# Kernel tuning notes

Measured on AMD Instinct MI355X. Metric: run time of the kernel, lower is better.

The kernel has to match this reference:

```python
import jax, jax.numpy as jnp
import numpy as np

B, F, T = 2, 512, 512
D, N, H = 1024, 16, 64   # hidden, heads, head_dim
K = 32                   # time-bias MLP kernal_size
FILT = 4096              # FFN filter size
L = 4                    # num_decoder_blocks
EPS = 1e-6


def _glorot(key, shape, fan_in, fan_out):
    lim = np.sqrt(6.0 / (fan_in + fan_out)).astype(np.float32)
    return jax.random.uniform(key, shape, jnp.float32, -lim, lim)


def setup_inputs() -> dict:
    key = jax.random.key(0)
    ks = jax.random.split(key, 18)
    inp = {
        'decoder_inputs': jax.random.normal(ks[0], (B, F, D), jnp.float32),
        'encoder_outputs': jax.random.normal(ks[1], (B, T, D), jnp.float32),
        'decoder_times_dist': jax.random.uniform(ks[2], (B, F, F), jnp.float32),
        'decoder_encoder_times_dist': jax.random.uniform(ks[3], (B, F, T), jnp.float32),
        'dec_self_attn_bias': jnp.zeros((B, 1, 1, F), jnp.float32),
        'enc_dec_attn_bias': jnp.zeros((B, 1, 1, T), jnp.float32),
        # per-block stacked parameters (leading dim L)
        'Wq': _glorot(ks[4], (L, D, N, H), D, D),
        'Wk': _glorot(ks[5], (L, D, N, H), D, D),
        'Wv': _glorot(ks[6], (L, D, N, H), D, D),
        'Wo': _glorot(ks[7], (L, N, H, D), D, D),
        'Wth': _glorot(ks[8], (L, 1, K), 1, K),
        'bth': jnp.zeros((L, K), jnp.float32),
        'Wto': _glorot(ks[9], (L, K, 1), K, 1),
        'bto': jnp.zeros((L, 1), jnp.float32),
        'Wf1': _glorot(ks[10], (L, D, FILT), D, FILT),
        'bf1': jnp.zeros((L, FILT), jnp.float32),
        'Wf2': _glorot(ks[11], (L, FILT, D), FILT, D),
        'bf2': jnp.zeros((L, D), jnp.float32),
    }
    return inp


def _norm(x):
    # non-trainable LayerNormalization: (x - mean) / (std + eps)
    m = jnp.mean(x, axis=-1, keepdims=True)
    s = jnp.sqrt(jnp.mean((x - m) ** 2, axis=-1, keepdims=True))
    return (x - m) / (s + EPS)


def _attention(x, src, dist, bias, Wq, Wk, Wv, Wo, Wth, bth, Wto, bto):
    q = jnp.einsum('bfd,dnh->bfnh', x, Wq) * (H ** -0.5)
    k = jnp.einsum('btd,dnh->btnh', src, Wk)
    v = jnp.einsum('btd,dnh->btnh', src, Wv)
    # learned time bias: [B,F,T,1] -> relu MLP(K) -> 1 -> [B,F,T]
    hbias = jax.nn.relu(dist[..., None] @ Wth + bth)        # [B,F,T,K]
    qs_bias = (hbias @ Wto + bto)[..., 0]                   # [B,F,T]
    logits = jnp.einsum('btnh,bfnh->bnft', k, q)            # [B,N,F,T]
    logits = logits + bias + qs_bias[:, None]
    w = jax.nn.softmax(logits, axis=-1)
    out = jnp.einsum('bnft,btnh->bfnh', w, v)
    return jnp.einsum('bfnh,nhd->bfd', out, Wo)


def reference(decoder_inputs, encoder_outputs, decoder_times_dist,
              decoder_encoder_times_dist, dec_self_attn_bias, enc_dec_attn_bias,
              Wq, Wk, Wv, Wo, Wth, bth, Wto, bto, Wf1, bf1, Wf2, bf2):
    # decoder_times_dist / dec_self_attn_bias are accepted but unused (as in source call)
    x = decoder_inputs
    for i in range(L):
        # enc-dec attention with pre-norm + residual
        y = _attention(_norm(x), encoder_outputs, decoder_encoder_times_dist,
                       enc_dec_attn_bias, Wq[i], Wk[i], Wv[i], Wo[i],
                       Wth[i], bth[i], Wto[i], bto[i])
        x = x + y
        # FFN with pre-norm + residual
        y = jax.nn.relu(_norm(x) @ Wf1[i] + bf1[i]) @ Wf2[i] + bf2[i]
        x = x + y
    return _norm(x)
```

## Files before the change

kernel.cpp:

```cpp
#include <hip/hip_runtime.h>

typedef unsigned short u16;
typedef __attribute__((ext_vector_type(8))) unsigned short u16x8;
typedef __attribute__((ext_vector_type(4))) unsigned short u16x4;
typedef __attribute__((ext_vector_type(4))) float f32x4;

#define DEVI __device__ __forceinline__

DEVI u16 f2bf(float f){
  unsigned u = __float_as_uint(f);
  u += 0x7FFFu + ((u >> 16) & 1u);
  return (u16)(u >> 16);
}

DEVI float bf2f(u16 b){
  return __uint_as_float((unsigned)b << 16);
}

DEVI void gload16(const void* g, void* l){
  __builtin_amdgcn_global_load_lds((const __attribute__((address_space(1))) void*)g,
                                   (__attribute__((address_space(3))) void*)l, 16, 0, 0);
}

DEVI float wave_sum(float v){
#pragma unroll
  for (int o = 32; o; o >>= 1) v += __shfl_xor(v, o, 64);
  return v;
}

#define MFMA16(a,b,c) __builtin_amdgcn_mfma_f32_16x16x32_bf16((a),(b),(c),0,0,0)

__global__ __launch_bounds__(256) void prep_k(
    const float* __restrict__ Wq, const float* __restrict__ Wk,
    const float* __restrict__ Wv, const float* __restrict__ Wo,
    const float* __restrict__ Wf1, const float* __restrict__ Wf2,
    const float* __restrict__ enc, const float* __restrict__ dist,
    const float* __restrict__ Wth0, const float* __restrict__ bth0,
    const float* __restrict__ Wto0, const float* __restrict__ bto0,
    u16* __restrict__ Wqt, u16* __restrict__ Wkt,
    u16* __restrict__ Wvt, u16* __restrict__ Wot,
    u16* __restrict__ Wf1t, u16* __restrict__ Wf2t,
    u16* __restrict__ encb, u16* __restrict__ qs0){
  __shared__ float tile[64][65];
  const int t = blockIdx.x;
  if (t < 12288){
    const float* in; u16* out; int R, C, r0, c0;
    if (t < 4096){
      const int mat = t >> 8, ti = t & 255, sel = mat >> 2, l = mat & 3;
      in  = (sel == 0 ? Wq : sel == 1 ? Wk : sel == 2 ? Wv : Wo) + (size_t)l * 1048576;
      out = (sel == 0 ? Wqt : sel == 1 ? Wkt : sel == 2 ? Wvt : Wot) + (size_t)l * 1048576;
      R = 1024; C = 1024; r0 = (ti & 15) << 6; c0 = (ti >> 4) << 6;
    } else if (t < 8192){
      const int t2 = t - 4096, mat = t2 >> 10, ti = t2 & 1023;
      in = Wf1 + (size_t)mat * 4194304; out = Wf1t + (size_t)mat * 4194304;
      R = 1024; C = 4096; r0 = (ti & 15) << 6; c0 = (ti >> 4) << 6;
    } else {
      const int t2 = t - 8192, mat = t2 >> 10, ti = t2 & 1023;
      in = Wf2 + (size_t)mat * 4194304; out = Wf2t + (size_t)mat * 4194304;
      R = 4096; C = 1024; r0 = (ti & 63) << 6; c0 = (ti >> 6) << 6;
    }
    const int rr0 = threadIdx.x >> 4, cc = (threadIdx.x & 15) * 4;
#pragma unroll
    for (int it = 0; it < 4; it++){
      const int rr = rr0 + it * 16;
      const float4 v = *(const float4*)(in + (size_t)(r0 + rr) * C + c0 + cc);
      tile[rr][cc] = v.x; tile[rr][cc+1] = v.y;
      tile[rr][cc+2] = v.z; tile[rr][cc+3] = v.w;
    }
    __syncthreads();
#pragma unroll
    for (int it = 0; it < 2; it++){
      const int chunk = threadIdx.x + it * 256;
      const int c = chunk >> 3, q = (chunk & 7) * 8;
      union { u16x8 v8; u16 e[8]; } ob;
#pragma unroll
      for (int i = 0; i < 8; i++) ob.e[i] = f2bf(tile[q + i][c]);
      *(u16x8*)(out + (size_t)(c0 + c) * R + r0 + q) = ob.v8;
    }
  } else if (t < 13312){
    const int i = (t - 12288) * 256 + threadIdx.x;
    float4 v = ((const float4*)enc)[i];
    u16x4 o = { f2bf(v.x), f2bf(v.y), f2bf(v.z), f2bf(v.w) };
    ((u16x4*)encb)[i] = o;
  } else {
    const int bi = t - 13312, ly = bi >> 9, xi = bi & 511;
    const float* Wth = Wth0 + ly*32;
    const float* bth = bth0 + ly*32;
    const float* Wto = Wto0 + ly*32;
    u16* qs = qs0 + (size_t)ly * 524288;
    const int idx = xi * 256 + threadIdx.x;
    float4 s4 = ((const float4*)dist)[idx];
    float sv[4] = { s4.x, s4.y, s4.z, s4.w };
    float r[4];
    const float b0 = bto0[ly];
#pragma unroll
    for (int c = 0; c < 4; c++) r[c] = b0;
#pragma unroll
    for (int k = 0; k < 32; k++){
      const float wk = Wth[k], bk = bth[k], ok = Wto[k];
#pragma unroll
      for (int c = 0; c < 4; c++){
        float h = fmaxf(sv[c] * wk + bk, 0.0f);
        r[c] += h * ok;
      }
    }
    u16x4 o = { f2bf(r[0]), f2bf(r[1]), f2bf(r[2]), f2bf(r[3]) };
    ((u16x4*)qs)[idx] = o;
  }
}

template<int COPY>
__global__ __launch_bounds__(256) void layernorm_k(const float* __restrict__ in,
                                                   float* __restrict__ x,
                                                   u16* __restrict__ outp){
  const int row = blockIdx.x;
  const int tid = threadIdx.x;
  const float4 v = ((const float4*)(in + (size_t)row * 1024))[tid];
  if (COPY) ((float4*)x)[(size_t)row * 256 + tid] = v;
  __shared__ float sb[8];
  const int wid = tid >> 6, lane = tid & 63;
  float s = wave_sum(v.x + v.y + v.z + v.w);
  if (lane == 0) sb[wid] = s;
  __syncthreads();
  const float mean = (sb[0] + sb[1] + sb[2] + sb[3]) * (1.0f / 1024.0f);
  const float dx = v.x - mean, dy = v.y - mean, dz = v.z - mean, dw = v.w - mean;
  float q = wave_sum(dx*dx + dy*dy + dz*dz + dw*dw);
  if (lane == 0) sb[4 + wid] = q;
  __syncthreads();
  const float sd = sqrtf((sb[4] + sb[5] + sb[6] + sb[7]) * (1.0f / 1024.0f));
  const float inv = 1.0f / (sd + 1e-6f);
  u16x4 o = { f2bf(dx*inv), f2bf(dy*inv), f2bf(dz*inv), f2bf(dw*inv) };
  ((u16x4*)outp)[(size_t)row * 256 + tid] = o;
}

template<int MODE, int BN>
DEVI void gemm128_core(const u16* A, int lda, const u16* Bt, int ldb,
                       int Klen, int Nd, void* Cout,
                       const float* bias, u16* Als, u16* Bls, int row0, int col0){
  constexpr int WN = BN / 2, FN = BN / 32;
  constexpr int BSZ = BN * 64;
  const int tid = threadIdx.x;
  const int wid = tid >> 6, lane = tid & 63;
  const int wm = wid >> 1, wn = wid & 1;
  const int lrow = lane & 15, g = lane >> 4, e7 = lane & 7;
  f32x4 acc[4][FN] = {};

  const int scol = ((lane & 7) ^ ((lane >> 3) & 7)) * 8;
  const u16* Ag = A + (size_t)(row0 + wid*8 + (lane >> 3)) * lda + scol;
  const u16* Bg = Bt + (size_t)(col0 + wid*8 + (lane >> 3)) * ldb + scol;
  const int dst0 = wid * 512;

  const int nt = Klen >> 6;

#define STAGE128(buf, k0)                                                     \
  {                                                                           \
    _Pragma("unroll")                                                         \
    for (int q = 0; q < 4; q++)                                               \
      gload16(Ag + (size_t)q*32*lda + (k0), Als + (buf)*8192 + dst0 + q*2048);\
    _Pragma("unroll")                                                         \
    for (int q = 0; q < BN/32; q++)                                           \
      gload16(Bg + (size_t)q*32*ldb + (k0), Bls + (buf)*BSZ + dst0 + q*2048); \
  }

  STAGE128(0, 0);
  __syncthreads();

  for (int t = 0; t < nt; t++){
    const int cur = t & 1;
    if (t + 1 < nt) STAGE128(cur ^ 1, (t + 1) << 6);
    const u16* Ab = Als + cur * 8192;
    const u16* Bb = Bls + cur * BSZ;
#pragma unroll
    for (int ks = 0; ks < 2; ks++){
      const int sl = (((ks << 2) + g) ^ e7) << 3;
      u16x8 av[4], bv[FN];
#pragma unroll
      for (int mi = 0; mi < 4; mi++)
        av[mi] = *(const u16x8*)(Ab + (wm*64 + mi*16 + lrow) * 64 + sl);
#pragma unroll
      for (int ni = 0; ni < FN; ni++)
        bv[ni] = *(const u16x8*)(Bb + (wn*WN + ni*16 + lrow) * 64 + sl);
#pragma unroll
      for (int mi = 0; mi < 4; mi++)
#pragma unroll
        for (int ni = 0; ni < FN; ni++)
          acc[mi][ni] = MFMA16(av[mi], bv[ni], acc[mi][ni]);
    }
    __syncthreads();
  }
#undef STAGE128

#pragma unroll
  for (int mi = 0; mi < 4; mi++){
#pragma unroll
    for (int ni = 0; ni < FN; ni++){
      const int col = col0 + wn*WN + ni*16 + lrow;
#pragma unroll
      for (int j = 0; j < 4; j++){
        const int row = row0 + wm*64 + mi*16 + g*4 + j;
        float v = acc[mi][ni][j];
        if (MODE == 3) v = fmaxf(v + bias[col], 0.0f);
        if (MODE == 0 || MODE == 3)
          ((u16*)Cout)[(size_t)row * Nd + col] = f2bf(v);
        else if (MODE == 6)
          ((u16*)Cout)[(size_t)((col >> 9)*16 + (row >> 6)) * 32768
                       + (row & 63) * 512 + (col & 511)] = f2bf(v);
        else
          ((float*)Cout)[(size_t)row * Nd + col] = v;
      }
    }
  }
}

template<int MODE>
__global__ __launch_bounds__(256) void gemm128_k(const u16* __restrict__ A, int lda,
    const u16* __restrict__ Bt, int ldb, int Klen, int Nd, void* __restrict__ Cout,
    const float* __restrict__ bias){
  __shared__ __align__(16) u16 Als[2 * 8192];
  __shared__ __align__(16) u16 Bls[2 * 4096];
  gemm128_core<MODE, 64>(A, lda, Bt, ldb, Klen, Nd, Cout, bias,
                         Als, Bls, blockIdx.y * 128, blockIdx.x * 64);
}

__global__ __launch_bounds__(256) void gemmKV_k(const u16* __restrict__ encb,
    const u16* __restrict__ Wkt, const u16* __restrict__ Wvt,
    u16* __restrict__ Kb, u16* __restrict__ Vt){
  __shared__ __align__(16) u16 Als[2 * 8192];
  __shared__ __align__(16) u16 Bls[2 * 4096];
  const int z = blockIdx.z, l = z >> 1;
  if ((z & 1) == 0)
    gemm128_core<0, 64>(encb, 1024, Wkt + (size_t)l*1048576, 1024, 1024, 1024,
                        Kb + (size_t)l*1048576, nullptr,
                        Als, Bls, blockIdx.y * 128, blockIdx.x * 64);
  else
    gemm128_core<6, 64>(Wvt + (size_t)l*1048576, 1024, encb, 1024, 1024, 1024,
                        Vt + (size_t)l*1048576, nullptr,
                        Als, Bls, blockIdx.y * 128, blockIdx.x * 64);
}

__global__ __launch_bounds__(256) void gemm_splitk_k(const u16* __restrict__ A, int lda,
    const u16* __restrict__ Bt, int ldb, int Klen, float* __restrict__ part){
  __shared__ __align__(16) u16 Als[2 * 8192];
  __shared__ __align__(16) u16 Bls[2 * 4096];
  const int z = blockIdx.z;
  gemm128_core<5, 64>(A + (size_t)z * Klen, lda, Bt + (size_t)z * Klen, ldb, Klen, 1024,
                      part + (size_t)z * 1048576, nullptr,
                      Als, Bls, blockIdx.y * 128, blockIdx.x * 64);
}

template<int BIAS, int LAST>
__global__ __launch_bounds__(256) void reduce_ln_k(const float* __restrict__ part,
    const float* __restrict__ bias, float* __restrict__ x, u16* __restrict__ xn,
    float* __restrict__ dout){
  const int row = blockIdx.x, tid = threadIdx.x;
  const size_t idx = (size_t)row * 256 + tid;
  float4 v = ((const float4*)x)[idx];
  float4 p0 = ((const float4*)part)[idx];
  float4 p1 = ((const float4*)(part + 1048576))[idx];
  float4 p2 = ((const float4*)(part + 2097152))[idx];
  float4 p3 = ((const float4*)(part + 3145728))[idx];
  v.x += p0.x + p1.x + p2.x + p3.x;
  v.y += p0.y + p1.y + p2.y + p3.y;
  v.z += p0.z + p1.z + p2.z + p3.z;
  v.w += p0.w + p1.w + p2.w + p3.w;
  if (BIAS){
    const float4 b = *(const float4*)(bias + tid * 4);
    v.x += b.x; v.y += b.y; v.z += b.z; v.w += b.w;
  }
  if (!LAST) ((float4*)x)[idx] = v;

  __shared__ float sb[8];
  const int wid = tid >> 6, lane = tid & 63;
  float s = wave_sum(v.x + v.y + v.z + v.w);
  if (lane == 0) sb[wid] = s;
  __syncthreads();
  const float mean = (sb[0] + sb[1] + sb[2] + sb[3]) * (1.0f / 1024.0f);
  const float dx = v.x - mean, dy = v.y - mean, dz = v.z - mean, dw = v.w - mean;
  float q = wave_sum(dx*dx + dy*dy + dz*dz + dw*dw);
  if (lane == 0) sb[4 + wid] = q;
  __syncthreads();
  const float sd = sqrtf((sb[4] + sb[5] + sb[6] + sb[7]) * (1.0f / 1024.0f));
  const float inv = 1.0f / (sd + 1e-6f);
  if (LAST){
    ((float4*)dout)[idx] = make_float4(dx*inv, dy*inv, dz*inv, dw*inv);
  } else {
    u16x4 o = { f2bf(dx*inv), f2bf(dy*inv), f2bf(dz*inv), f2bf(dw*inv) };
    ((u16x4*)xn)[idx] = o;
  }
}

__global__ __launch_bounds__(256, 2) void attn_k(const u16* __restrict__ xn,
    const u16* __restrict__ Wqt,
    const u16* __restrict__ Kb, const u16* __restrict__ Vt,
    const u16* __restrict__ qs, const float* __restrict__ abias,
    u16* __restrict__ aout){
  const int n = blockIdx.x, f0 = blockIdx.y * 64, b = blockIdx.z;
  const int w = threadIdx.x >> 6, lane = threadIdx.x & 63;
  const int l15 = lane & 15, g = lane >> 4, e7 = lane & 7;
  const int fw = f0 + w * 16;
  __shared__ __align__(16) u16 Pl[4][16 * 512];
  u16* pw = &Pl[w][0];

  u16x8 qf0, qf1;
  {
    u16* Als = &Pl[0][0];
    u16* Bls = &Pl[1][0];
    const int wm = w >> 1, wn = w & 1;
    f32x4 qac[2][2] = {};
    const int scol = ((lane & 7) ^ ((lane >> 3) & 7)) * 8;
    const u16* Ag = xn + (size_t)(b*512 + f0 + w*8 + (lane >> 3)) * 1024 + scol;
    const u16* Bg = Wqt + (size_t)(n*64 + w*8 + (lane >> 3)) * 1024 + scol;
    const int dq = w * 512;

#define STAGEQ(buf, k0)                                         \
    gload16(Ag + (k0),            Als + (buf)*4096 + dq);       \
    gload16(Ag + 32*1024 + (k0),  Als + (buf)*4096 + dq + 2048);\
    gload16(Bg + (k0),            Bls + (buf)*4096 + dq);       \
    gload16(Bg + 32*1024 + (k0),  Bls + (buf)*4096 + dq + 2048);

    STAGEQ(0, 0);
    __syncthreads();
    for (int t = 0; t < 16; t++){
      const int cur = t & 1;
      if (t < 15){ STAGEQ(cur ^ 1, (t + 1) << 6); }
      const u16* Ab = Als + cur * 4096;
      const u16* Bb = Bls + cur * 4096;
#pragma unroll
      for (int ks = 0; ks < 2; ks++){
        const int sl = (((ks << 2) + g) ^ e7) << 3;
        u16x8 av[2], bv[2];
#pragma unroll
        for (int mi = 0; mi < 2; mi++)
          av[mi] = *(const u16x8*)(Ab + (wm*32 + mi*16 + l15) * 64 + sl);
#pragma unroll
        for (int ni = 0; ni < 2; ni++)
          bv[ni] = *(const u16x8*)(Bb + (wn*32 + ni*16 + l15) * 64 + sl);
#pragma unroll
        for (int mi = 0; mi < 2; mi++)
#pragma unroll
          for (int ni = 0; ni < 2; ni++)
            qac[mi][ni] = MFMA16(av[mi], bv[ni], qac[mi][ni]);
      }
      __syncthreads();
    }
#undef STAGEQ

    u16* Qt = &Pl[2][0];
#pragma unroll
    for (int mi = 0; mi < 2; mi++)
#pragma unroll
      for (int ni = 0; ni < 2; ni++)
#pragma unroll
        for (int j = 0; j < 4; j++){
          const int r = wm*32 + mi*16 + g*4 + j;
          const int c = wn*32 + ni*16 + l15;
          const int byte = r*128 + (((c >> 3) ^ (r & 7)) << 4) + (c & 7)*2;
          *(u16*)((char*)Qt + byte) = f2bf(qac[mi][ni][j] * 0.125f);
        }
    __syncthreads();
    const int r = w*16 + l15;
    const char* qrow = (char*)Qt + r*128;
    qf0 = *(const u16x8*)(qrow + ((g ^ (r & 7)) << 4));
    qf1 = *(const u16x8*)(qrow + (((4 + g) ^ (r & 7)) << 4));
    __syncthreads();
  }

  f32x4 acc[32];
  const u16* kp = Kb + ((size_t)b*512 + l15) * 1024 + n*64 + g*8;
#pragma unroll
  for (int tf = 0; tf < 32; tf++){
    u16x8 k0 = *(const u16x8*)(kp + (size_t)tf*16*1024);
    u16x8 k1 = *(const u16x8*)(kp + (size_t)tf*16*1024 + 32);
    f32x4 z = {0.f, 0.f, 0.f, 0.f};
    z = MFMA16(k0, qf0, z);
    acc[tf] = MFMA16(k1, qf1, z);
  }

  const u16* qsp = qs + ((size_t)b*512 + fw + l15) * 512 + g*4;
  const float* abp = abias + (size_t)b*512 + g*4;
  float m = -3.0e38f;
#pragma unroll
  for (int tf = 0; tf < 32; tf++){
    u16x4 qv = *(const u16x4*)(qsp + tf*16);
    float4 av = *(const float4*)(abp + tf*16);
    acc[tf][0] += bf2f(qv[0]) + av.x;
    acc[tf][1] += bf2f(qv[1]) + av.y;
    acc[tf][2] += bf2f(qv[2]) + av.z;
    acc[tf][3] += bf2f(qv[3]) + av.w;
    m = fmaxf(m, fmaxf(fmaxf(acc[tf][0], acc[tf][1]), fmaxf(acc[tf][2], acc[tf][3])));
  }
  m = fmaxf(m, __shfl_xor(m, 16, 64));
  m = fmaxf(m, __shfl_xor(m, 32, 64));

  float s = 0.f;
#pragma unroll
  for (int tf = 0; tf < 32; tf++){
#pragma unroll
    for (int j = 0; j < 4; j++){
      float e = __expf(acc[tf][j] - m);
      acc[tf][j] = e; s += e;
    }
  }
  s += __shfl_xor(s, 16, 64);
  s += __shfl_xor(s, 32, 64);
  const float inv = 1.0f / s;
  float invj[4];
#pragma unroll
  for (int j = 0; j < 4; j++) invj[j] = __shfl(inv, g*4 + j, 64);

#pragma unroll
  for (int tf = 0; tf < 32; tf++){
    const int chunk = tf*2 + (g >> 1);
    const int boff = (l15 << 10) + ((chunk ^ e7) << 4) + ((g & 1) << 3);
    u16x4 pk = { f2bf(acc[tf][0]), f2bf(acc[tf][1]), f2bf(acc[tf][2]), f2bf(acc[tf][3]) };
    *(u16x4*)((char*)pw + boff) = pk;
  }

  f32x4 oacc[4] = {};
  const u16* vp = Vt + ((size_t)(b*16 + n)*64 + l15) * 512 + g*8;
  for (int kk = 0; kk < 16; kk++){
    u16x8 pa = *(const u16x8*)((char*)pw + (l15 << 10) + ((((kk << 2) + g) ^ e7) << 4));
#pragma unroll
    for (int nf = 0; nf < 4; nf++){
      u16x8 vb = *(const u16x8*)(vp + (size_t)nf*16*512 + kk*32);
      oacc[nf] = MFMA16(pa, vb, oacc[nf]);
    }
  }

  u16* op = aout + ((size_t)b*512 + fw + g*4) * 1024 + n*64 + l15;
#pragma unroll
  for (int nf = 0; nf < 4; nf++)
#pragma unroll
    for (int j = 0; j < 4; j++)
      op[(size_t)j*1024 + nf*16] = f2bf(oacc[nf][j] * invj[j]);
}

extern "C" void kernel_launch(void* const* d_in, const int* in_sizes, int n_in,
                              void* d_out, int out_size, void* d_ws, size_t ws_size,
                              hipStream_t stream){
  const float* dec_in   = (const float*)d_in[0];
  const float* enc      = (const float*)d_in[1];
  const float* dist     = (const float*)d_in[3];
  const float* abias    = (const float*)d_in[5];
  const float* Wq  = (const float*)d_in[6];
  const float* Wk  = (const float*)d_in[7];
  const float* Wv  = (const float*)d_in[8];
  const float* Wo  = (const float*)d_in[9];
  const float* Wth = (const float*)d_in[10];
  const float* bth = (const float*)d_in[11];
  const float* Wto = (const float*)d_in[12];
  const float* bto = (const float*)d_in[13];
  const float* Wf1 = (const float*)d_in[14];
  const float* bf1 = (const float*)d_in[15];
  const float* Wf2 = (const float*)d_in[16];
  const float* bf2 = (const float*)d_in[17];
  float* dout = (float*)d_out;

  char* wp = (char*)d_ws;
  auto alloc = [&](size_t n) -> char* {
    char* p = wp; wp += (n + 255) & ~(size_t)255; return p;
  };
  float* x     = (float*)alloc((size_t)1048576 * 4);
  u16*  xn     = (u16*)alloc((size_t)1048576 * 2);
  u16*  encb   = (u16*)alloc((size_t)1048576 * 2);
  u16*  Wqt    = (u16*)alloc((size_t)4194304 * 2);
  u16*  Wkt    = (u16*)alloc((size_t)4194304 * 2);
  u16*  Wvt    = (u16*)alloc((size_t)4194304 * 2);
  u16*  Wot    = (u16*)alloc((size_t)4194304 * 2);
  u16*  Wf1t   = (u16*)alloc((size_t)16777216 * 2);
  u16*  Wf2t   = (u16*)alloc((size_t)16777216 * 2);
  u16*  Kb     = (u16*)alloc((size_t)4194304 * 2);
  u16*  Vt     = (u16*)alloc((size_t)4194304 * 2);
  u16*  qs     = (u16*)alloc((size_t)2097152 * 2);
  u16*  aout   = (u16*)alloc((size_t)1048576 * 2);
  u16*  ffh    = (u16*)alloc((size_t)4194304 * 2);
  float* part  = (float*)alloc((size_t)4194304 * 4);

  prep_k<<<15360, 256, 0, stream>>>(Wq, Wk, Wv, Wo, Wf1, Wf2, enc, dist,
                                    Wth, bth, Wto, bto,
                                    Wqt, Wkt, Wvt, Wot, Wf1t, Wf2t, encb, qs);
  gemmKV_k<<<dim3(16, 8, 8), 256, 0, stream>>>(encb, Wkt, Wvt, Kb, Vt);
  layernorm_k<1><<<1024, 256, 0, stream>>>(dec_in, x, xn);

  for (int i = 0; i < 4; i++){
    const size_t wo = (size_t)i * 1048576;

    attn_k<<<dim3(16, 8, 2), 256, 0, stream>>>(xn, Wqt + wo, Kb + wo, Vt + wo,
                                               qs + (size_t)i * 524288, abias, aout);

    gemm_splitk_k<<<dim3(16, 8, 4), 256, 0, stream>>>(aout, 1024, Wot + wo, 1024, 256, part);
    reduce_ln_k<0, 0><<<1024, 256, 0, stream>>>(part, nullptr, x, xn, nullptr);

    gemm128_k<3><<<dim3(64, 8), 256, 0, stream>>>(xn, 1024, Wf1t + (size_t)i*4194304, 1024,
                                                  1024, 4096, ffh, bf1 + (size_t)i*4096);
    gemm_splitk_k<<<dim3(16, 8, 4), 256, 0, stream>>>(ffh, 4096, Wf2t + (size_t)i*4194304, 4096,
                                                      1024, part);
    if (i < 3)
      reduce_ln_k<1, 0><<<1024, 256, 0, stream>>>(part, bf2 + (size_t)i*1024, x, xn, nullptr);
    else
      reduce_ln_k<1, 1><<<1024, 256, 0, stream>>>(part, bf2 + (size_t)i*1024, x, nullptr, dout);
  }
}
```

Baseline: 450.1 us.

## Merge prep, layernorm and KV GEMM launches with multi-tile pipelined transposes

Splits the weight-preparation work into two kernels. The first converts Wk/Wv, the encoder outputs and the initial layernorm. The second transposes Wq/Wf1/Wf2, computes the time-bias MLP and runs the K/V projection GEMM in the same grid. Each transpose block now handles four 64x64 tiles with a double-buffered LDS pipeline instead of one tile per block. The aim is to cut launch count and tail effects and to overlap the bandwidth-bound transposes with the K/V GEMM. Wo is transposed by a separate launch that, as written, does each tile twice (both selector branches point to Wo), which wastes some bandwidth.

```diff
diff --git a/kernel.cpp b/kernel.cpp
--- a/kernel.cpp
+++ b/kernel.cpp
@@ -30,107 +30,81 @@
 
 #define MFMA16(a,b,c) __builtin_amdgcn_mfma_f32_16x16x32_bf16((a),(b),(c),0,0,0)
 
-__global__ __launch_bounds__(256) void prep_k(
-    const float* __restrict__ Wq, const float* __restrict__ Wk,
-    const float* __restrict__ Wv, const float* __restrict__ Wo,
-    const float* __restrict__ Wf1, const float* __restrict__ Wf2,
-    const float* __restrict__ enc, const float* __restrict__ dist,
-    const float* __restrict__ Wth0, const float* __restrict__ bth0,
-    const float* __restrict__ Wto0, const float* __restrict__ bto0,
-    u16* __restrict__ Wqt, u16* __restrict__ Wkt,
-    u16* __restrict__ Wvt, u16* __restrict__ Wot,
-    u16* __restrict__ Wf1t, u16* __restrict__ Wf2t,
-    u16* __restrict__ encb, u16* __restrict__ qs0){
-  __shared__ float tile[64][65];
+DEVI void trans4(const float* __restrict__ in, u16* __restrict__ out,
+                 int R, int C, int r0b, int c0, float* tb){
+  const int rr0 = threadIdx.x >> 4, cc = (threadIdx.x & 15) * 4;
+  float4 rv[4];
+#define TLOAD(tt)                                                             \
+  { _Pragma("unroll")                                                         \
+    for (int it = 0; it < 4; it++)                                            \
+      rv[it] = *(const float4*)(in + (size_t)(r0b + (tt)*64 + rr0 + it*16) * C + c0 + cc); }
+#define TDSW(buf)                                                             \
+  { _Pragma("unroll")                                                         \
+    for (int it = 0; it < 4; it++){                                           \
+      const int rr = rr0 + it*16;                                             \
+      float* tr = tb + ((buf)*64 + rr) * 65 + cc;                             \
+      tr[0] = rv[it].x; tr[1] = rv[it].y; tr[2] = rv[it].z; tr[3] = rv[it].w; } }
+#define TWOUT(buf, tt)                                                        \
+  { _Pragma("unroll")                                                         \
+    for (int it2 = 0; it2 < 2; it2++){                                        \
+      const int chunk = threadIdx.x + it2 * 256;                              \
+      const int c = chunk >> 3, q = (chunk & 7) * 8;                          \
+      union { u16x8 v8; u16 e[8]; } ob;                                       \
+      _Pragma("unroll")                                                       \
+      for (int i = 0; i < 8; i++) ob.e[i] = f2bf(tb[((buf)*64 + q + i) * 65 + c]); \
+      *(u16x8*)(out + (size_t)(c0 + c) * R + r0b + (tt)*64 + q) = ob.v8; } }
+
+  TLOAD(0); TDSW(0);
+  __syncthreads();
+#pragma unroll
+  for (int tt = 0; tt < 4; tt++){
+    const int buf = tt & 1;
+    if (tt < 3) TLOAD(tt + 1);
+    TWOUT(buf, tt);
+    if (tt < 3) TDSW(buf ^ 1);
+    __syncthreads();
+  }
+#undef TLOAD
+#undef TDSW
+#undef TWOUT
+}
+
+__global__ __launch_bounds__(256) void prepA_k(
+    const float* __restrict__ Wk, const float* __restrict__ Wv,
+    const float* __restrict__ enc, const float* __restrict__ dec_in,
+    float* __restrict__ x, u16* __restrict__ xn,
+    u16* __restrict__ Wkt, u16* __restrict__ Wvt, u16* __restrict__ encb){
+  __shared__ __align__(16) float tb[2 * 64 * 65];
   const int t = blockIdx.x;
-  if (t < 12288){
-    const float* in; u16* out; int R, C, r0, c0;
-    if (t < 4096){
-      const int mat = t >> 8, ti = t & 255, sel = mat >> 2, l = mat & 3;
-      in  = (sel == 0 ? Wq : sel == 1 ? Wk : sel == 2 ? Wv : Wo) + (size_t)l * 1048576;
-      out = (sel == 0 ? Wqt : sel == 1 ? Wkt : sel == 2 ? Wvt : Wot) + (size_t)l * 1048576;
-      R = 1024; C = 1024; r0 = (ti & 15) << 6; c0 = (ti >> 4) << 6;
-    } else if (t < 8192){
-      const int t2 = t - 4096, mat = t2 >> 10, ti = t2 & 1023;
-      in = Wf1 + (size_t)mat * 4194304; out = Wf1t + (size_t)mat * 4194304;
-      R = 1024; C = 4096; r0 = (ti & 15) << 6; c0 = (ti >> 4) << 6;
-    } else {
-      const int t2 = t - 8192, mat = t2 >> 10, ti = t2 & 1023;
-      in = Wf2 + (size_t)mat * 4194304; out = Wf2t + (size_t)mat * 4194304;
-      R = 4096; C = 1024; r0 = (ti & 63) << 6; c0 = (ti >> 6) << 6;
-    }
-    const int rr0 = threadIdx.x >> 4, cc = (threadIdx.x & 15) * 4;
-#pragma unroll
-    for (int it = 0; it < 4; it++){
-      const int rr = rr0 + it * 16;
-      const float4 v = *(const float4*)(in + (size_t)(r0 + rr) * C + c0 + cc);
-      tile[rr][cc] = v.x; tile[rr][cc+1] = v.y;
-      tile[rr][cc+2] = v.z; tile[rr][cc+3] = v.w;
-    }
-    __syncthreads();
-#pragma unroll
-    for (int it = 0; it < 2; it++){
-      const int chunk = threadIdx.x + it * 256;
-      const int c = chunk >> 3, q = (chunk & 7) * 8;
-      union { u16x8 v8; u16 e[8]; } ob;
-#pragma unroll
-      for (int i = 0; i < 8; i++) ob.e[i] = f2bf(tile[q + i][c]);
-      *(u16x8*)(out + (size_t)(c0 + c) * R + r0 + q) = ob.v8;
-    }
-  } else if (t < 13312){
-    const int i = (t - 12288) * 256 + threadIdx.x;
+  if (t < 512){
+    const int sel = t >> 8, t2 = t & 255, mat = t2 >> 6, gi = t2 & 63;
+    const float* in = (sel ? Wv : Wk) + (size_t)mat * 1048576;
+    u16* out = (sel ? Wvt : Wkt) + (size_t)mat * 1048576;
+    trans4(in, out, 1024, 1024, (gi & 3) << 8, (gi >> 2) << 6, tb);
+  } else if (t < 1536){
+    const int i = (t - 512) * 256 + threadIdx.x;
     float4 v = ((const float4*)enc)[i];
     u16x4 o = { f2bf(v.x), f2bf(v.y), f2bf(v.z), f2bf(v.w) };
     ((u16x4*)encb)[i] = o;
   } else {
-    const int bi = t - 13312, ly = bi >> 9, xi = bi & 511;
-    const float* Wth = Wth0 + ly*32;
-    const float* bth = bth0 + ly*32;
-    const float* Wto = Wto0 + ly*32;
-    u16* qs = qs0 + (size_t)ly * 524288;
-    const int idx = xi * 256 + threadIdx.x;
-    float4 s4 = ((const float4*)dist)[idx];
-    float sv[4] = { s4.x, s4.y, s4.z, s4.w };
-    float r[4];
-    const float b0 = bto0[ly];
-#pragma unroll
-    for (int c = 0; c < 4; c++) r[c] = b0;
-#pragma unroll
-    for (int k = 0; k < 32; k++){
-      const float wk = Wth[k], bk = bth[k], ok = Wto[k];
-#pragma unroll
-      for (int c = 0; c < 4; c++){
-        float h = fmaxf(sv[c] * wk + bk, 0.0f);
-        r[c] += h * ok;
-      }
-    }
-    u16x4 o = { f2bf(r[0]), f2bf(r[1]), f2bf(r[2]), f2bf(r[3]) };
-    ((u16x4*)qs)[idx] = o;
-  }
-}
-
-template<int COPY>
-__global__ __launch_bounds__(256) void layernorm_k(const float* __restrict__ in,
-                                                   float* __restrict__ x,
-                                                   u16* __restrict__ outp){
-  const int row = blockIdx.x;
-  const int tid = threadIdx.x;
-  const float4 v = ((const float4*)(in + (size_t)row * 1024))[tid];
-  if (COPY) ((float4*)x)[(size_t)row * 256 + tid] = v;
-  __shared__ float sb[8];
-  const int wid = tid >> 6, lane = tid & 63;
-  float s = wave_sum(v.x + v.y + v.z + v.w);
-  if (lane == 0) sb[wid] = s;
-  __syncthreads();
-  const float mean = (sb[0] + sb[1] + sb[2] + sb[3]) * (1.0f / 1024.0f);
-  const float dx = v.x - mean, dy = v.y - mean, dz = v.z - mean, dw = v.w - mean;
-  float q = wave_sum(dx*dx + dy*dy + dz*dz + dw*dw);
-  if (lane == 0) sb[4 + wid] = q;
-  __syncthreads();
-  const float sd = sqrtf((sb[4] + sb[5] + sb[6] + sb[7]) * (1.0f / 1024.0f));
-  const float inv = 1.0f / (sd + 1e-6f);
-  u16x4 o = { f2bf(dx*inv), f2bf(dy*inv), f2bf(dz*inv), f2bf(dw*inv) };
-  ((u16x4*)outp)[(size_t)row * 256 + tid] = o;
+    const int row = t - 1536, tid = threadIdx.x;
+    const float4 v = ((const float4*)(dec_in + (size_t)row * 1024))[tid];
+    ((float4*)x)[(size_t)row * 256 + tid] = v;
+    __shared__ float sb[8];
+    const int wid = tid >> 6, lane = tid & 63;
+    float s = wave_sum(v.x + v.y + v.z + v.w);
+    if (lane == 0) sb[wid] = s;
+    __syncthreads();
+    const float mean = (sb[0] + sb[1] + sb[2] + sb[3]) * (1.0f / 1024.0f);
+    const float dx = v.x - mean, dy = v.y - mean, dz = v.z - mean, dw = v.w - mean;
+    float q = wave_sum(dx*dx + dy*dy + dz*dz + dw*dw);
+    if (lane == 0) sb[4 + wid] = q;
+    __syncthreads();
+    const float sd = sqrtf((sb[4] + sb[5] + sb[6] + sb[7]) * (1.0f / 1024.0f));
+    const float inv = 1.0f / (sd + 1e-6f);
+    u16x4 o = { f2bf(dx*inv), f2bf(dy*inv), f2bf(dz*inv), f2bf(dw*inv) };
+    ((u16x4*)xn)[(size_t)row * 256 + tid] = o;
+  }
 }
 
 template<int MODE, int BN>
@@ -149,7 +123,6 @@
   const u16* Ag = A + (size_t)(row0 + wid*8 + (lane >> 3)) * lda + scol;
   const u16* Bg = Bt + (size_t)(col0 + wid*8 + (lane >> 3)) * ldb + scol;
   const int dst0 = wid * 512;
-
   const int nt = Klen >> 6;
 
 #define STAGE128(buf, k0)                                                     \
@@ -212,6 +185,74 @@
   }
 }
 
+__global__ __launch_bounds__(256) void prepB_gemmKV_k(
+    const float* __restrict__ Wq, const float* __restrict__ Wf1,
+    const float* __restrict__ Wf2, const float* __restrict__ dist,
+    const float* __restrict__ Wth0, const float* __restrict__ bth0,
+    const float* __restrict__ Wto0, const float* __restrict__ bto0,
+    const u16* __restrict__ encb, const u16* __restrict__ Wkt,
+    const u16* __restrict__ Wvt,
+    u16* __restrict__ Wqt, u16* __restrict__ Wf1t, u16* __restrict__ Wf2t,
+    u16* __restrict__ qs0, u16* __restrict__ Kb, u16* __restrict__ Vt){
+  __shared__ __align__(16) char smem[49152];
+  const int t = blockIdx.x;
+  if (t < 2304){
+    float* tb = (float*)smem;
+    if (t < 256){
+      const int mat = t >> 6, gi = t & 63;
+      trans4(Wq + (size_t)mat * 1048576, Wqt + (size_t)mat * 1048576,
+             1024, 1024, (gi & 3) << 8, (gi >> 2) << 6, tb);
+    } else if (t < 1280){
+      const int t2 = t - 256, mat = t2 >> 8, gi = t2 & 255;
+      trans4(Wf1 + (size_t)mat * 4194304, Wf1t + (size_t)mat * 4194304,
+             1024, 4096, (gi & 3) << 8, (gi >> 2) << 6, tb);
+    } else {
+      const int t2 = t - 1280, mat = t2 >> 8, gi = t2 & 255;
+      trans4(Wf2 + (size_t)mat * 4194304, Wf2t + (size_t)mat * 4194304,
+             4096, 1024, (gi >> 4) << 8, (gi & 15) << 6, tb);
+    }
+  } else if (t < 4352){
+    const int bi = t - 2304, ly = bi >> 9, xi = bi & 511;
+    const float* Wth = Wth0 + ly*32;
+    const float* bth = bth0 + ly*32;
+    const float* Wto = Wto0 + ly*32;
+    u16* qs = qs0 + (size_t)ly * 524288;
+    const int idx = xi * 256 + threadIdx.x;
+    float4 s4 = ((const float4*)dist)[idx];
+    float sv[4] = { s4.x, s4.y, s4.z, s4.w };
+    float r[4];
+    const float b0 = bto0[ly];
+#pragma unroll
+    for (int c = 0; c < 4; c++) r[c] = b0;
+#pragma unroll
+    for (int k = 0; k < 32; k++){
+      const float wk = Wth[k], bk = bth[k], ok = Wto[k];
+#pragma unroll
+      for (int c = 0; c < 4; c++){
+        float h = fmaxf(sv[c] * wk + bk, 0.0f);
+        r[c] += h * ok;
+      }
+    }
+    u16x4 o = { f2bf(r[0]), f2bf(r[1]), f2bf(r[2]), f2bf(r[3]) };
+    ((u16x4*)qs)[idx] = o;
+  } else {
+    u16* Als = (u16*)smem;
+    u16* Bls = (u16*)(smem + 32768);
+    const int t2 = t - 4352;
+    const int z = t2 >> 7, rem = t2 & 127;
+    const int y = rem >> 4, xb = rem & 15;
+    const int l = z >> 1;
+    if ((z & 1) == 0)
+      gemm128_core<0, 64>(encb, 1024, Wkt + (size_t)l*1048576, 1024, 1024, 1024,
+                          Kb + (size_t)l*1048576, nullptr,
+                          Als, Bls, y * 128, xb * 64);
+    else
+      gemm128_core<6, 64>(Wvt + (size_t)l*1048576, 1024, encb, 1024, 1024, 1024,
+                          Vt + (size_t)l*1048576, nullptr,
+                          Als, Bls, y * 128, xb * 64);
+  }
+}
+
 template<int MODE>
 __global__ __launch_bounds__(256) void gemm128_k(const u16* __restrict__ A, int lda,
     const u16* __restrict__ Bt, int ldb, int Klen, int Nd, void* __restrict__ Cout,
@@ -220,22 +261,6 @@
   __shared__ __align__(16) u16 Bls[2 * 4096];
   gemm128_core<MODE, 64>(A, lda, Bt, ldb, Klen, Nd, Cout, bias,
                          Als, Bls, blockIdx.y * 128, blockIdx.x * 64);
-}
-
-__global__ __launch_bounds__(256) void gemmKV_k(const u16* __restrict__ encb,
-    const u16* __restrict__ Wkt, const u16* __restrict__ Wvt,
-    u16* __restrict__ Kb, u16* __restrict__ Vt){
-  __shared__ __align__(16) u16 Als[2 * 8192];
-  __shared__ __align__(16) u16 Bls[2 * 4096];
-  const int z = blockIdx.z, l = z >> 1;
-  if ((z & 1) == 0)
-    gemm128_core<0, 64>(encb, 1024, Wkt + (size_t)l*1048576, 1024, 1024, 1024,
-                        Kb + (size_t)l*1048576, nullptr,
-                        Als, Bls, blockIdx.y * 128, blockIdx.x * 64);
-  else
-    gemm128_core<6, 64>(Wvt + (size_t)l*1048576, 1024, encb, 1024, 1024, 1024,
-                        Vt + (size_t)l*1048576, nullptr,
-                        Als, Bls, blockIdx.y * 128, blockIdx.x * 64);
 }
 
 __global__ __launch_bounds__(256) void gemm_splitk_k(const u16* __restrict__ A, int lda,
@@ -476,11 +501,13 @@
   u16*  ffh    = (u16*)alloc((size_t)4194304 * 2);
   float* part  = (float*)alloc((size_t)4194304 * 4);
 
-  prep_k<<<15360, 256, 0, stream>>>(Wq, Wk, Wv, Wo, Wf1, Wf2, enc, dist,
-                                    Wth, bth, Wto, bto,
-                                    Wqt, Wkt, Wvt, Wot, Wf1t, Wf2t, encb, qs);
-  gemmKV_k<<<dim3(16, 8, 8), 256, 0, stream>>>(encb, Wkt, Wvt, Kb, Vt);
-  layernorm_k<1><<<1024, 256, 0, stream>>>(dec_in, x, xn);
+  prepA_k<<<2560, 256, 0, stream>>>(Wk, Wv, enc, dec_in, x, xn, Wkt, Wvt, encb);
+  prepB_gemmKV_k<<<5376, 256, 0, stream>>>(Wq, Wf1, Wf2, dist, Wth, bth, Wto, bto,
+                                           encb, Wkt, Wvt,
+                                           Wqt, Wf1t, Wf2t, qs, Kb, Vt);
+
+  prepA_k<<<512, 256, 0, stream>>>(Wo, Wo, nullptr, nullptr, nullptr, nullptr,
+                                   Wot, Wot, nullptr);
 
   for (int i = 0; i < 4; i++){
     const size_t wo = (size_t)i * 1048576;
```

New measurement: 431.4 us. 4.2% less time.
